# Performance work log

Hardware: AMD Instinct MI355X
Metric: run time of the kernel (lower is better)

Reference implementation:

```python
import jax, jax.numpy as jnp
import numpy as np

# dims / hyperparams (mirror init_kwargs)
B, N, C, K = 256, 16000, 32, 64          # batch, samples, cochlear channels, gammatone taps
FS, FMIN, FMAX, BWF = 16000, 100.0, 8000.0, 1.0
WINDOW, STRIDE = 256, 128                # inner hair cell framing -> T = 124
ANS, HID, OUT = 10, 50, 10               # auditory-nerve fanout, bushy/ic hidden, AC out
BETA, THR = 0.95, 1.0                    # snn.Leaky(beta=0.95), threshold 1.0, subtract reset
AN_LO, AN_HI, AN_THR = 0.5, 1.5, 0.5     # an_range scales + AN firing threshold

# Heaviside spike with ATan surrogate gradient (snntorch default style)
@jax.custom_vjp
def spike(u):
    return (u > 0).astype(u.dtype)

def _spike_fwd(u):
    return spike(u), u

def _spike_bwd(u, g):
    return (g / (1.0 + (jnp.pi * u) ** 2),)

spike.defvjp(_spike_fwd, _spike_bwd)

def _gammatone_bank():
    # ERB-spaced 4th-order gammatone impulse responses, unit L2 norm. [C, K]
    def hz2erb(f):
        return 21.4 * np.log10(1.0 + 0.00437 * f)
    def erb2hz(e):
        return (10.0 ** (e / 21.4) - 1.0) / 0.00437
    cfs = erb2hz(np.linspace(hz2erb(FMIN), hz2erb(FMAX), C))
    b = BWF * 1.019 * 24.7 * (4.37 * cfs / 1000.0 + 1.0)
    t = np.arange(K) / FS
    ker = (t[None, :] ** 3) * np.exp(-2 * np.pi * b[:, None] * t[None, :]) \
          * np.cos(2 * np.pi * cfs[:, None] * t[None, :])
    ker = ker / (np.linalg.norm(ker, axis=1, keepdims=True) + 1e-12)
    return jnp.asarray(ker, jnp.float32)

def setup_inputs() -> dict:
    key = jax.random.key(0)
    k1, k2, k3, k4 = jax.random.split(key, 4)
    audio = jax.random.normal(k1, (B, N), dtype=jnp.float32)
    W_bushy = jax.random.normal(k2, (HID, C * ANS), dtype=jnp.float32) / np.sqrt(C * ANS)
    W_ic = jax.random.normal(k3, (HID, HID), dtype=jnp.float32) / np.sqrt(HID)
    W_ac = jax.random.normal(k4, (OUT, HID), dtype=jnp.float32) / np.sqrt(HID)
    return {"audio": audio, "gt_kernels": _gammatone_bank(),
            "W_bushy": W_bushy, "W_ic": W_ic, "W_ac": W_ac}

def reference(audio, gt_kernels, W_bushy, W_ic, W_ac):
    # Cochlear: gammatone filterbank, [B,1,N] conv [C,1,K] SAME -> [B,C,N]
    y = jax.lax.conv_general_dilated(audio[:, None, :], gt_kernels[:, None, :],
                                     window_strides=(1,), padding="SAME")
    # InnerHairCell: half-wave rectify + moving-average framing -> [B,C,T]
    y = jnp.maximum(y, 0.0)
    env = jax.lax.reduce_window(y, 0.0, jax.lax.add,
                                (1, 1, WINDOW), (1, 1, STRIDE), "VALID") / WINDOW
    frames = jnp.transpose(env, (2, 0, 1))  # [T,B,C]
    scales = jnp.linspace(AN_LO, AN_HI, ANS, dtype=jnp.float32)

    def lif(mem, cur):
        mem = BETA * mem + cur
        spk = spike(mem - THR)
        return spk, mem - THR * spk  # subtract reset

    def step(carry, x_t):  # x_t [B,C]
        mem_b, mem_ic, mem_ac = carry
        # AuditoryNerve: ans scaled copies per channel, threshold fire -> [B, C*ANS]
        spk_an = spike(x_t[:, :, None] * scales - AN_THR).reshape(x_t.shape[0], -1)
        spk_b, mem_b = lif(mem_b, spk_an @ W_bushy.T)     # Bushy
        spk_ic, mem_ic = lif(mem_ic, spk_b @ W_ic.T)      # InferiorColliculus
        spk_ac, mem_ac = lif(mem_ac, spk_ic @ W_ac.T)     # AudioCortex
        return (mem_b, mem_ic, mem_ac), (spk_ac, mem_ac)

    bsz = audio.shape[0]
    init = (jnp.zeros((bsz, HID), audio.dtype),
            jnp.zeros((bsz, HID), audio.dtype),
            jnp.zeros((bsz, OUT), audio.dtype))
    _, (spk_rec, mem_rec) = jax.lax.scan(step, init, frames)
    # stack along dim=1 as in torch code -> [B,T,OUT]
    return jnp.transpose(spk_rec, (1, 0, 2)), jnp.transpose(mem_rec, (1, 0, 2))
```

## Files before the change

kernel.cpp:

```cpp
#include <hip/hip_runtime.h>

#define B_   256
#define N_   16000
#define C_   32
#define K_   64
#define T_   124
#define NJ   125
#define HID_ 50
#define OUT_ 10
#define TB_  1024

typedef unsigned int u32;
typedef float v2f __attribute__((ext_vector_type(2)));
struct __align__(16) f2x2 { v2f lo, hi; };

__device__ __forceinline__ float fadd(float a, float b) { return __fadd_rn(a, b); }
__device__ __forceinline__ float fmul(float a, float b) { return __fmul_rn(a, b); }
__device__ __forceinline__ float fsub(float a, float b) { return __fsub_rn(a, b); }

__device__ __forceinline__ void PKFMA(v2f& y, v2f a, const f2x2& T, int k) {
    switch (k) {
    case 0:  asm("v_pk_fma_f32 %0, %1, %2, %0 op_sel:[0,0,0] op_sel_hi:[1,0,1]"
                 : "+v"(y) : "v"(a), "v"(T.lo)); break;
    case 1:  asm("v_pk_fma_f32 %0, %1, %2, %0 op_sel:[0,1,0] op_sel_hi:[1,1,1]"
                 : "+v"(y) : "v"(a), "v"(T.lo)); break;
    case 2:  asm("v_pk_fma_f32 %0, %1, %2, %0 op_sel:[0,0,0] op_sel_hi:[1,0,1]"
                 : "+v"(y) : "v"(a), "v"(T.hi)); break;
    default: asm("v_pk_fma_f32 %0, %1, %2, %0 op_sel:[0,1,0] op_sel_hi:[1,1,1]"
                 : "+v"(y) : "v"(a), "v"(T.hi)); break;
    }
}

__global__ __launch_bounds__(256, 4) void convA(const float* __restrict__ audio,
                                                const float* __restrict__ gt,
                                                float* __restrict__ Sg) {
    __shared__ __align__(16) float abI[1280];
    __shared__ __align__(16) float kLDS[C_ * K_];
    __shared__ __align__(16) float ybuf[4][4][264];

    const int b = blockIdx.x, g = blockIdx.y;
    const int tid = threadIdx.x, w = tid >> 6, lane = tid & 63;
    const float* arow = audio + (size_t)b * N_;

    const int origin = (g << 10) - 32;
    for (int idx = tid; idx < 1280; idx += 256) {
        int P = idx / 640, j = idx - P * 640;
        int ii = j >> 1, h = j & 1;
        int gi = origin + (P << 9) + (h << 8) + ii;
        float v = (gi >= 0 && gi < N_) ? arow[gi] : 0.0f;
        abI[P * 640 + (j ^ (((j >> 5) & 1) << 2))] = v;
    }
    for (int i = tid; i < C_ * K_; i += 256) kLDS[i] = gt[i];
    __syncthreads();

    for (int G = 0; G < 2; ++G) {
        const float* kgrp = &kLDS[((w << 3) + (G << 2)) << 6];

        v2f Y[2][4][4];
#pragma unroll
        for (int P = 0; P < 2; ++P)
#pragma unroll
            for (int ch = 0; ch < 4; ++ch)
#pragma unroll
                for (int d = 0; d < 4; ++d) { Y[P][ch][d].x = 0.0f; Y[P][ch][d].y = 0.0f; }

        f2x2 Tp[4];

        {
            f2x2 Tc[4];
#pragma unroll
            for (int ch = 0; ch < 4; ++ch)
                Tc[ch] = *(const f2x2*)(kgrp + (ch << 6));
            const int u = lane;
            const int p1 = (u << 3) ^ (((u >> 2) & 1) << 2);
#pragma unroll
            for (int P = 0; P < 2; ++P) {
                const float* abP = abI + P * 640;
                const f2x2 A0 = *(const f2x2*)(abP + p1);
                const f2x2 A1 = *(const f2x2*)(abP + (p1 ^ 4));
#pragma unroll
                for (int e = 0; e < 4; ++e) {
                    const v2f a = (e == 0) ? A0.lo : (e == 1) ? A0.hi
                                : (e == 2) ? A1.lo : A1.hi;
#pragma unroll
                    for (int ch = 0; ch < 4; ++ch)
#pragma unroll
                        for (int d = 0; d < 4; ++d) {
                            const int kb = e - 1 - d;
                            if (kb >= 0) PKFMA(Y[P][ch][d], a, Tc[ch], kb);
                        }
                }
            }
#pragma unroll
            for (int ch = 0; ch < 4; ++ch) Tp[ch] = Tc[ch];
        }

#pragma unroll 1
        for (int q = 1; q < 16; ++q) {
            f2x2 Tc[4];
#pragma unroll
            for (int ch = 0; ch < 4; ++ch)
                Tc[ch] = *(const f2x2*)(kgrp + (ch << 6) + (q << 2));
            const int u = lane + q;
            const int p1 = (u << 3) ^ (((u >> 2) & 1) << 2);
#pragma unroll
            for (int P = 0; P < 2; ++P) {
                const float* abP = abI + P * 640;
                const f2x2 A0 = *(const f2x2*)(abP + p1);
                const f2x2 A1 = *(const f2x2*)(abP + (p1 ^ 4));
#pragma unroll
                for (int e = 0; e < 4; ++e) {
                    const v2f a = (e == 0) ? A0.lo : (e == 1) ? A0.hi
                                : (e == 2) ? A1.lo : A1.hi;
#pragma unroll
                    for (int ch = 0; ch < 4; ++ch)
#pragma unroll
                        for (int d = 0; d < 4; ++d) {
                            const int ts = e - 1 - d;
                            if (ts >= 0) PKFMA(Y[P][ch][d], a, Tc[ch], ts);
                            else         PKFMA(Y[P][ch][d], a, Tp[ch], 4 + ts);
                        }
                }
            }
#pragma unroll
            for (int ch = 0; ch < 4; ++ch) Tp[ch] = Tc[ch];
        }

        {
            const int u = lane + 16;
            const int p1 = (u << 3) ^ (((u >> 2) & 1) << 2);
#pragma unroll
            for (int P = 0; P < 2; ++P) {
                const float* abP = abI + P * 640;
                const f2x2 A0 = *(const f2x2*)(abP + p1);
                const f2x2 A1 = *(const f2x2*)(abP + (p1 ^ 4));
#pragma unroll
                for (int e = 0; e < 4; ++e) {
                    const v2f a = (e == 0) ? A0.lo : (e == 1) ? A0.hi
                                : (e == 2) ? A1.lo : A1.hi;
#pragma unroll
                    for (int ch = 0; ch < 4; ++ch)
#pragma unroll
                        for (int d = 0; d < 4; ++d) {
                            const int ts = e - 1 - d;
                            if (ts < 0) PKFMA(Y[P][ch][d], a, Tp[ch], 4 + ts);
                        }
                }
            }
        }

#pragma unroll
        for (int pp = 0; pp < 4; ++pp) {
            const int P = pp >> 1, h = pp & 1;
#pragma unroll
            for (int ch = 0; ch < 4; ++ch) {
                float4 z;
                z.x = fmaxf(h ? Y[P][ch][0].y : Y[P][ch][0].x, 0.0f);
                z.y = fmaxf(h ? Y[P][ch][1].y : Y[P][ch][1].x, 0.0f);
                z.z = fmaxf(h ? Y[P][ch][2].y : Y[P][ch][2].x, 0.0f);
                z.w = fmaxf(h ? Y[P][ch][3].y : Y[P][ch][3].x, 0.0f);
                *(float4*)(&ybuf[w][ch][((lane >> 5) * 132) + ((lane & 31) << 2)]) = z;
            }
            {
                const int ch2 = lane >> 4, blk = (lane >> 3) & 1, j = lane & 7;
                const float* yb = &ybuf[w][ch2][blk * 132 + j];
                float r = yb[0];
#pragma unroll
                for (int m = 1; m < 16; ++m) r = fadd(r, yb[m << 3]);
                float v = fadd(r, __shfl_xor(r, 1));
                v = fadd(v, __shfl_xor(v, 2));
                v = fadd(v, __shfl_xor(v, 4));
                const int jg = (g << 3) + (pp << 1) + blk;
                const int c = (w << 3) + (G << 2) + ch2;
                if (j == 0 && jg < NJ) Sg[((size_t)b * C_ + c) * NJ + jg] = v;
            }
        }
    }
}

__global__ __launch_bounds__(TB_, 1) void snnB(const float* __restrict__ Sg,
                                               const float* __restrict__ Wb,
                                               const float* __restrict__ Wic,
                                               const float* __restrict__ Wac,
                                               float* __restrict__ out) {
    __shared__ float sWb[HID_ * 321];
    __shared__ float sWic[HID_ * 51];
    __shared__ float sWac[OUT_ * 51];
    __shared__ u32   mask[T_ * 10];
    __shared__ float cur[T_ * HID_];
    __shared__ float icur[T_ * HID_];
    __shared__ float acur[T_ * 12];

    const int b = blockIdx.x, tid = threadIdx.x;

    for (int i = tid; i < HID_ * 320; i += TB_) {
        int r = i / 320;
        sWb[r * 321 + (i - r * 320)] = Wb[i];
    }
    for (int i = tid; i < HID_ * HID_; i += TB_) {
        int r = i / 50;
        sWic[r * 51 + (i - r * 50)] = Wic[i];
    }
    for (int i = tid; i < OUT_ * HID_; i += TB_) {
        int r = i / 50;
        sWac[r * 51 + (i - r * 50)] = Wac[i];
    }

    const float* Sb = Sg + (size_t)b * C_ * NJ;
    for (int idx = tid; idx < T_ * 10; idx += TB_) {
        int t = idx / 10, wd = idx - t * 10;
        u32 m = 0;
        int c_prev = -1;
        float env = 0.0f;
        for (int k = 0; k < 32; ++k) {
            int i = wd * 32 + k;
            int c = i / 10, s = i - c * 10;
            if (c != c_prev) {
                env = fmul(fadd(Sb[c * NJ + t], Sb[c * NJ + t + 1]), 0.00390625f);
                c_prev = c;
            }
            float sf = (s == 9) ? 1.5f : (float)(0.5 + (double)s * (1.0 / 9.0));
            if (fsub(fmul(env, sf), 0.5f) > 0.0f) m |= (1u << k);
        }
        mask[idx] = m;
    }
    __syncthreads();

    for (int k = tid; k < 31 * HID_; k += TB_) {
        int t0 = k / 50, h = k - t0 * 50;
        const float* wr = sWb + h * 321;
        const u32* m0 = mask + (t0     ) * 10;
        const u32* m1 = mask + (t0 + 31) * 10;
        const u32* m2 = mask + (t0 + 62) * 10;
        const u32* m3 = mask + (t0 + 93) * 10;
        float a0 = 0.0f, a1 = 0.0f, a2 = 0.0f, a3 = 0.0f;
#pragma unroll 8
        for (int i = 0; i < 320; ++i) {
            float wv = wr[i];
            const int wi = i >> 5, sh = i & 31;
            a0 = fadd(a0, ((m0[wi] >> sh) & 1u) ? wv : 0.0f);
            a1 = fadd(a1, ((m1[wi] >> sh) & 1u) ? wv : 0.0f);
            a2 = fadd(a2, ((m2[wi] >> sh) & 1u) ? wv : 0.0f);
            a3 = fadd(a3, ((m3[wi] >> sh) & 1u) ? wv : 0.0f);
        }
        cur[(t0     ) * 50 + h] = a0;
        cur[(t0 + 31) * 50 + h] = a1;
        cur[(t0 + 62) * 50 + h] = a2;
        cur[(t0 + 93) * 50 + h] = a3;
    }
    __syncthreads();

    if (tid < HID_) {
        float mem = 0.0f;
        for (int t = 0; t < T_; ++t) {
            float m = fadd(fmul(0.95f, mem), cur[t * 50 + tid]);
            float sp = (fsub(m, 1.0f) > 0.0f) ? 1.0f : 0.0f;
            mem = fsub(m, sp);
            cur[t * 50 + tid] = sp;
        }
    }
    __syncthreads();

    for (int idx = tid; idx < T_ * HID_; idx += TB_) {
        int t = idx / 50, h = idx - t * 50;
        const float* wr = sWic + h * 51;
        const float* sb = cur + t * 50;
        float acc = 0.0f;
#pragma unroll
        for (int g = 0; g < HID_; ++g) acc = fadd(acc, fmul(sb[g], wr[g]));
        icur[idx] = acc;
    }
    __syncthreads();

    if (tid < HID_) {
        float mem = 0.0f;
        for (int t = 0; t < T_; ++t) {
            float m = fadd(fmul(0.95f, mem), icur[t * 50 + tid]);
            float sp = (fsub(m, 1.0f) > 0.0f) ? 1.0f : 0.0f;
            mem = fsub(m, sp);
            icur[t * 50 + tid] = sp;
        }
    }
    __syncthreads();

    for (int idx = tid; idx < T_ * OUT_; idx += TB_) {
        int t = idx / 10, o = idx - t * 10;
        const float* wr = sWac + o * 51;
        const float* sb = icur + t * 50;
        float acc = 0.0f;
#pragma unroll
        for (int g = 0; g < HID_; ++g) acc = fadd(acc, fmul(sb[g], wr[g]));
        acur[t * 12 + o] = acc;
    }
    __syncthreads();

    if (tid < OUT_) {
        float mem = 0.0f;
        for (int t = 0; t < T_; ++t) {
            float m = fadd(fmul(0.95f, mem), acur[t * 12 + tid]);
            float sp = (fsub(m, 1.0f) > 0.0f) ? 1.0f : 0.0f;
            float mo = fsub(m, sp);
            mem = mo;
            size_t base = ((size_t)b * T_ + t) * OUT_ + tid;
            out[base] = sp;
            out[(size_t)(B_ * T_ * OUT_) + base] = mo;
        }
    }
}

extern "C" void kernel_launch(void* const* d_in, const int* in_sizes, int n_in,
                              void* d_out, int out_size, void* d_ws, size_t ws_size,
                              hipStream_t stream) {
    (void)in_sizes; (void)n_in; (void)out_size; (void)ws_size;
    const float* audio = (const float*)d_in[0];
    const float* gt    = (const float*)d_in[1];
    const float* Wb    = (const float*)d_in[2];
    const float* Wic   = (const float*)d_in[3];
    const float* Wac   = (const float*)d_in[4];

    float* Sg = (float*)d_ws;

    convA<<<dim3(B_, 16), dim3(256), 0, stream>>>(audio, gt, Sg);
    snnB<<<dim3(B_), dim3(TB_), 0, stream>>>(Sg, Wb, Wic, Wac, (float*)d_out);
}
```

Measured before the change: 333.6 us.

## Move gammatone taps to scalar registers and restructure SNN bushy accumulation

In the conv kernel, filter taps are read through wave-uniform pointers so they can sit in scalar registers as the v_pk_fma operand. This removes the kernel LDS buffer and the carried previous-tap registers, and the launch bound rises to 6 blocks per CU. In the SNN kernel, the bushy-layer sum now has each thread handle 8 timesteps and select weights with a bit-field-extract mask instead of a branchy select. The IC and AC matvecs use float4 LDS loads with fmaf over padded 52-wide rows. Replacing separate mul and add with fmaf may change rounding relative to the reference, and forcing taps into SGPRs via the 's' constraint depends on the compiler proving them uniform.

Result: faster. 325.9 us (-2.3%).

```diff
diff --git a/kernel.cpp b/kernel.cpp
--- a/kernel.cpp
+++ b/kernel.cpp
@@ -9,6 +9,7 @@
 #define HID_ 50
 #define OUT_ 10
 #define TB_  1024
+#define CURS 52
 
 typedef unsigned int u32;
 typedef float v2f __attribute__((ext_vector_type(2)));
@@ -21,21 +22,20 @@
 __device__ __forceinline__ void PKFMA(v2f& y, v2f a, const f2x2& T, int k) {
     switch (k) {
     case 0:  asm("v_pk_fma_f32 %0, %1, %2, %0 op_sel:[0,0,0] op_sel_hi:[1,0,1]"
-                 : "+v"(y) : "v"(a), "v"(T.lo)); break;
+                 : "+v"(y) : "v"(a), "s"(T.lo)); break;
     case 1:  asm("v_pk_fma_f32 %0, %1, %2, %0 op_sel:[0,1,0] op_sel_hi:[1,1,1]"
-                 : "+v"(y) : "v"(a), "v"(T.lo)); break;
+                 : "+v"(y) : "v"(a), "s"(T.lo)); break;
     case 2:  asm("v_pk_fma_f32 %0, %1, %2, %0 op_sel:[0,0,0] op_sel_hi:[1,0,1]"
-                 : "+v"(y) : "v"(a), "v"(T.hi)); break;
+                 : "+v"(y) : "v"(a), "s"(T.hi)); break;
     default: asm("v_pk_fma_f32 %0, %1, %2, %0 op_sel:[0,1,0] op_sel_hi:[1,1,1]"
-                 : "+v"(y) : "v"(a), "v"(T.hi)); break;
+                 : "+v"(y) : "v"(a), "s"(T.hi)); break;
     }
 }
 
-__global__ __launch_bounds__(256, 4) void convA(const float* __restrict__ audio,
+__global__ __launch_bounds__(256, 6) void convA(const float* __restrict__ audio,
                                                 const float* __restrict__ gt,
                                                 float* __restrict__ Sg) {
     __shared__ __align__(16) float abI[1280];
-    __shared__ __align__(16) float kLDS[C_ * K_];
     __shared__ __align__(16) float ybuf[4][4][264];
 
     const int b = blockIdx.x, g = blockIdx.y;
@@ -50,11 +50,11 @@
         float v = (gi >= 0 && gi < N_) ? arow[gi] : 0.0f;
         abI[P * 640 + (j ^ (((j >> 5) & 1) << 2))] = v;
     }
-    for (int i = tid; i < C_ * K_; i += 256) kLDS[i] = gt[i];
     __syncthreads();
 
     for (int G = 0; G < 2; ++G) {
-        const float* kgrp = &kLDS[((w << 3) + (G << 2)) << 6];
+        const int rowbase = __builtin_amdgcn_readfirstlane(((w << 3) + (G << 2)) << 6);
+        const float* kg = gt + rowbase;
 
         v2f Y[2][4][4];
 #pragma unroll
@@ -63,14 +63,12 @@
             for (int ch = 0; ch < 4; ++ch)
 #pragma unroll
                 for (int d = 0; d < 4; ++d) { Y[P][ch][d].x = 0.0f; Y[P][ch][d].y = 0.0f; }
-
-        f2x2 Tp[4];
 
         {
             f2x2 Tc[4];
 #pragma unroll
             for (int ch = 0; ch < 4; ++ch)
-                Tc[ch] = *(const f2x2*)(kgrp + (ch << 6));
+                Tc[ch] = *(const f2x2*)(kg + (ch << 6));
             const int u = lane;
             const int p1 = (u << 3) ^ (((u >> 2) & 1) << 2);
 #pragma unroll
@@ -91,16 +89,16 @@
                         }
                 }
             }
-#pragma unroll
-            for (int ch = 0; ch < 4; ++ch) Tp[ch] = Tc[ch];
         }
 
 #pragma unroll 1
         for (int q = 1; q < 16; ++q) {
-            f2x2 Tc[4];
-#pragma unroll
-            for (int ch = 0; ch < 4; ++ch)
-                Tc[ch] = *(const f2x2*)(kgrp + (ch << 6) + (q << 2));
+            f2x2 Tm[4], Tc[4];
+#pragma unroll
+            for (int ch = 0; ch < 4; ++ch) {
+                Tm[ch] = *(const f2x2*)(kg + (ch << 6) + ((q - 1) << 2));
+                Tc[ch] = *(const f2x2*)(kg + (ch << 6) + (q << 2));
+            }
             const int u = lane + q;
             const int p1 = (u << 3) ^ (((u >> 2) & 1) << 2);
 #pragma unroll
@@ -118,15 +116,17 @@
                         for (int d = 0; d < 4; ++d) {
                             const int ts = e - 1 - d;
                             if (ts >= 0) PKFMA(Y[P][ch][d], a, Tc[ch], ts);
-                            else         PKFMA(Y[P][ch][d], a, Tp[ch], 4 + ts);
+                            else         PKFMA(Y[P][ch][d], a, Tm[ch], 4 + ts);
                         }
                 }
             }
-#pragma unroll
-            for (int ch = 0; ch < 4; ++ch) Tp[ch] = Tc[ch];
         }
 
         {
+            f2x2 Tm[4];
+#pragma unroll
+            for (int ch = 0; ch < 4; ++ch)
+                Tm[ch] = *(const f2x2*)(kg + (ch << 6) + 60);
             const int u = lane + 16;
             const int p1 = (u << 3) ^ (((u >> 2) & 1) << 2);
 #pragma unroll
@@ -143,7 +143,7 @@
 #pragma unroll
                         for (int d = 0; d < 4; ++d) {
                             const int ts = e - 1 - d;
-                            if (ts < 0) PKFMA(Y[P][ch][d], a, Tp[ch], 4 + ts);
+                            if (ts < 0) PKFMA(Y[P][ch][d], a, Tm[ch], 4 + ts);
                         }
                 }
             }
@@ -184,11 +184,11 @@
                                                const float* __restrict__ Wac,
                                                float* __restrict__ out) {
     __shared__ float sWb[HID_ * 321];
-    __shared__ float sWic[HID_ * 51];
-    __shared__ float sWac[OUT_ * 51];
-    __shared__ u32   mask[T_ * 10];
-    __shared__ float cur[T_ * HID_];
-    __shared__ float icur[T_ * HID_];
+    __shared__ __align__(16) float sWic[HID_ * 52];
+    __shared__ __align__(16) float sWac[OUT_ * 52];
+    __shared__ u32   mask[128 * 10];
+    __shared__ __align__(16) float cur[T_ * CURS];
+    __shared__ __align__(16) float icur[T_ * CURS];
     __shared__ float acur[T_ * 12];
 
     const int b = blockIdx.x, tid = threadIdx.x;
@@ -199,15 +199,16 @@
     }
     for (int i = tid; i < HID_ * HID_; i += TB_) {
         int r = i / 50;
-        sWic[r * 51 + (i - r * 50)] = Wic[i];
+        sWic[r * 52 + (i - r * 50)] = Wic[i];
     }
     for (int i = tid; i < OUT_ * HID_; i += TB_) {
         int r = i / 50;
-        sWac[r * 51 + (i - r * 50)] = Wac[i];
+        sWac[r * 52 + (i - r * 50)] = Wac[i];
     }
 
     const float* Sb = Sg + (size_t)b * C_ * NJ;
-    for (int idx = tid; idx < T_ * 10; idx += TB_) {
+    for (int idx = tid; idx < 1280; idx += TB_) {
+        if (idx >= T_ * 10) { mask[idx] = 0; continue; }
         int t = idx / 10, wd = idx - t * 10;
         u32 m = 0;
         int c_prev = -1;
@@ -226,70 +227,101 @@
     }
     __syncthreads();
 
-    for (int k = tid; k < 31 * HID_; k += TB_) {
-        int t0 = k / 50, h = k - t0 * 50;
+    if (tid < 16 * HID_) {
+        const int t0 = tid / 50, h = tid - t0 * 50;
         const float* wr = sWb + h * 321;
-        const u32* m0 = mask + (t0     ) * 10;
-        const u32* m1 = mask + (t0 + 31) * 10;
-        const u32* m2 = mask + (t0 + 62) * 10;
-        const u32* m3 = mask + (t0 + 93) * 10;
+        const u32* mrow = mask + t0 * 10;
         float a0 = 0.0f, a1 = 0.0f, a2 = 0.0f, a3 = 0.0f;
-#pragma unroll 8
-        for (int i = 0; i < 320; ++i) {
-            float wv = wr[i];
-            const int wi = i >> 5, sh = i & 31;
-            a0 = fadd(a0, ((m0[wi] >> sh) & 1u) ? wv : 0.0f);
-            a1 = fadd(a1, ((m1[wi] >> sh) & 1u) ? wv : 0.0f);
-            a2 = fadd(a2, ((m2[wi] >> sh) & 1u) ? wv : 0.0f);
-            a3 = fadd(a3, ((m3[wi] >> sh) & 1u) ? wv : 0.0f);
-        }
-        cur[(t0     ) * 50 + h] = a0;
-        cur[(t0 + 31) * 50 + h] = a1;
-        cur[(t0 + 62) * 50 + h] = a2;
-        cur[(t0 + 93) * 50 + h] = a3;
+        float a4 = 0.0f, a5 = 0.0f, a6 = 0.0f, a7 = 0.0f;
+#pragma unroll 1
+        for (int wi = 0; wi < 10; ++wi) {
+            const u32 w0 = mrow[wi], w1 = mrow[160 + wi];
+            const u32 w2 = mrow[320 + wi], w3 = mrow[480 + wi];
+            const u32 w4 = mrow[640 + wi], w5 = mrow[800 + wi];
+            const u32 w6 = mrow[960 + wi], w7 = mrow[1120 + wi];
+#pragma unroll
+            for (int b2 = 0; b2 < 32; ++b2) {
+                const float wv = wr[(wi << 5) + b2];
+                const int iw = __float_as_int(wv);
+                a0 = fadd(a0, __int_as_float(iw & __builtin_amdgcn_sbfe((int)w0, b2, 1)));
+                a1 = fadd(a1, __int_as_float(iw & __builtin_amdgcn_sbfe((int)w1, b2, 1)));
+                a2 = fadd(a2, __int_as_float(iw & __builtin_amdgcn_sbfe((int)w2, b2, 1)));
+                a3 = fadd(a3, __int_as_float(iw & __builtin_amdgcn_sbfe((int)w3, b2, 1)));
+                a4 = fadd(a4, __int_as_float(iw & __builtin_amdgcn_sbfe((int)w4, b2, 1)));
+                a5 = fadd(a5, __int_as_float(iw & __builtin_amdgcn_sbfe((int)w5, b2, 1)));
+                a6 = fadd(a6, __int_as_float(iw & __builtin_amdgcn_sbfe((int)w6, b2, 1)));
+                a7 = fadd(a7, __int_as_float(iw & __builtin_amdgcn_sbfe((int)w7, b2, 1)));
+            }
+        }
+        cur[(t0      ) * CURS + h] = a0;
+        cur[(t0 + 16 ) * CURS + h] = a1;
+        cur[(t0 + 32 ) * CURS + h] = a2;
+        cur[(t0 + 48 ) * CURS + h] = a3;
+        cur[(t0 + 64 ) * CURS + h] = a4;
+        cur[(t0 + 80 ) * CURS + h] = a5;
+        cur[(t0 + 96 ) * CURS + h] = a6;
+        if (t0 + 112 < T_) cur[(t0 + 112) * CURS + h] = a7;
     }
     __syncthreads();
 
     if (tid < HID_) {
         float mem = 0.0f;
         for (int t = 0; t < T_; ++t) {
-            float m = fadd(fmul(0.95f, mem), cur[t * 50 + tid]);
+            float m = fadd(fmul(0.95f, mem), cur[t * CURS + tid]);
             float sp = (fsub(m, 1.0f) > 0.0f) ? 1.0f : 0.0f;
             mem = fsub(m, sp);
-            cur[t * 50 + tid] = sp;
+            cur[t * CURS + tid] = sp;
         }
     }
     __syncthreads();
 
     for (int idx = tid; idx < T_ * HID_; idx += TB_) {
         int t = idx / 50, h = idx - t * 50;
-        const float* wr = sWic + h * 51;
-        const float* sb = cur + t * 50;
+        const float* wr = sWic + h * 52;
+        const float* sb = cur + t * CURS;
         float acc = 0.0f;
 #pragma unroll
-        for (int g = 0; g < HID_; ++g) acc = fadd(acc, fmul(sb[g], wr[g]));
-        icur[idx] = acc;
+        for (int g4 = 0; g4 < 12; ++g4) {
+            const float4 s4 = *(const float4*)(sb + (g4 << 2));
+            const float4 w4 = *(const float4*)(wr + (g4 << 2));
+            acc = fmaf(s4.x, w4.x, acc);
+            acc = fmaf(s4.y, w4.y, acc);
+            acc = fmaf(s4.z, w4.z, acc);
+            acc = fmaf(s4.w, w4.w, acc);
+        }
+        acc = fmaf(sb[48], wr[48], acc);
+        acc = fmaf(sb[49], wr[49], acc);
+        icur[t * CURS + h] = acc;
     }
     __syncthreads();
 
     if (tid < HID_) {
         float mem = 0.0f;
         for (int t = 0; t < T_; ++t) {
-            float m = fadd(fmul(0.95f, mem), icur[t * 50 + tid]);
+            float m = fadd(fmul(0.95f, mem), icur[t * CURS + tid]);
             float sp = (fsub(m, 1.0f) > 0.0f) ? 1.0f : 0.0f;
             mem = fsub(m, sp);
-            icur[t * 50 + tid] = sp;
+            icur[t * CURS + tid] = sp;
         }
     }
     __syncthreads();
 
     for (int idx = tid; idx < T_ * OUT_; idx += TB_) {
         int t = idx / 10, o = idx - t * 10;
-        const float* wr = sWac + o * 51;
-        const float* sb = icur + t * 50;
+        const float* wr = sWac + o * 52;
+        const float* sb = icur + t * CURS;
         float acc = 0.0f;
 #pragma unroll
-        for (int g = 0; g < HID_; ++g) acc = fadd(acc, fmul(sb[g], wr[g]));
+        for (int g4 = 0; g4 < 12; ++g4) {
+            const float4 s4 = *(const float4*)(sb + (g4 << 2));
+            const float4 w4 = *(const float4*)(wr + (g4 << 2));
+            acc = fmaf(s4.x, w4.x, acc);
+            acc = fmaf(s4.y, w4.y, acc);
+            acc = fmaf(s4.z, w4.z, acc);
+            acc = fmaf(s4.w, w4.w, acc);
+        }
+        acc = fmaf(sb[48], wr[48], acc);
+        acc = fmaf(sb[49], wr[49], acc);
         acur[t * 12 + o] = acc;
     }
     __syncthreads();
```
